# Optimization experiments

Measured on AMD Instinct MI355X. Metric: run time of the kernel, lower is better.

The kernel has to match this reference:

```python
import jax, jax.numpy as jnp
import numpy as np

B, L, D, H, DH, FF = 4, 1024, 1024, 16, 64, 4096
EPS = 1e-5


def _layer_norm(x, g, b):
    m = jnp.mean(x, -1, keepdims=True)
    v = jnp.mean((x - m) ** 2, -1, keepdims=True)
    return (x - m) * jax.lax.rsqrt(v + EPS) * g + b


def setup_inputs() -> dict:
    key = jax.random.key(0)
    ks = jax.random.split(key, 20)
    s = 0.02  # param init scale
    return {
        "x": jax.random.normal(ks[0], (B, L, D), jnp.float32),
        "adj_mask_matrix": jax.random.uniform(ks[1], (B * H, L, L), jnp.float32),
        "com_mask_matrix": jax.random.uniform(ks[2], (B * H, L, L), jnp.float32),
        "lattice_rel": jax.random.normal(ks[3], (2, 1, 1, DH), jnp.float32),
        "Wq": jax.random.normal(ks[4], (D, D), jnp.float32) * s,
        "bq": jnp.zeros((D,), jnp.float32),
        "Wk": jax.random.normal(ks[5], (D, D), jnp.float32) * s,
        "bk": jnp.zeros((D,), jnp.float32),
        "Wv": jax.random.normal(ks[6], (D, D), jnp.float32) * s,
        "bv": jnp.zeros((D,), jnp.float32),
        "Wo": jax.random.normal(ks[7], (D, D), jnp.float32) * s,
        "bo": jnp.zeros((D,), jnp.float32),
        "ln1_scale": jnp.ones((D,), jnp.float32),
        "ln1_bias": jnp.zeros((D,), jnp.float32),
        "W1": jax.random.normal(ks[8], (D, FF), jnp.float32) * s,
        "b1": jnp.zeros((FF,), jnp.float32),
        "W2": jax.random.normal(ks[9], (FF, D), jnp.float32) * s,
        "b2": jnp.zeros((D,), jnp.float32),
        "ln2_scale": jnp.ones((D,), jnp.float32),
        "ln2_bias": jnp.zeros((D,), jnp.float32),
    }


def reference(x, adj_mask_matrix, com_mask_matrix, lattice_rel,
              Wq, bq, Wk, bk, Wv, bv, Wo, bo, ln1_scale, ln1_bias,
              W1, b1, W2, b2, ln2_scale, ln2_bias):
    Bsz, Ln, Dm = x.shape
    # QKV projections; flat reshape [B,L,H*dh] -> [B*H,L,dh] matches torch .view
    Q = (x @ Wq + bq).reshape(Bsz * H, Ln, DH)
    K = (x @ Wk + bk).reshape(Bsz * H, Ln, DH)
    V = (x @ Wv + bv).reshape(Bsz * H, Ln, DH)
    scale = DH ** (-0.5)
    adj_rel = lattice_rel[0]  # [1,1,dh] broadcasts over (B*H, L)
    com_rel = lattice_rel[1]
    att_adj = jnp.einsum('bqd,bkd->bqk', Q + adj_rel, K + adj_rel) * scale
    att_com = jnp.einsum('bqd,bkd->bqk', Q + com_rel, K + com_rel) * scale
    # post-softmax multiplicative masking, then sum of the two attention maps
    mask_att = (jax.nn.softmax(att_adj, axis=-1) * adj_mask_matrix
                + jax.nn.softmax(att_com, axis=-1) * com_mask_matrix)
    context = jnp.matmul(mask_att, V).reshape(Bsz, Ln, H * DH)
    out = _layer_norm(context @ Wo + bo + x, ln1_scale, ln1_bias)
    ff = jax.nn.relu(out @ W1 + b1) @ W2 + b2
    return _layer_norm(ff + out, ln2_scale, ln2_bias)
```

## Files before the change

kernel.cpp:

```cpp
#include <hip/hip_runtime.h>

typedef __attribute__((ext_vector_type(8))) short s16x8;
typedef __attribute__((ext_vector_type(4))) float f32x4;
typedef unsigned short u16;
typedef unsigned int u32;

__device__ __forceinline__ u16 f2b(float f) {
    u32 u = __float_as_uint(f);
    u32 r = (u + 0x7fffu + ((u >> 16) & 1u)) >> 16;
    return (u16)r;
}

#define MFMA16(a, b, c) __builtin_amdgcn_mfma_f32_16x16x32_bf16(a, b, c, 0, 0, 0)
#define GLDS(gp, lp)                                                              \
    __builtin_amdgcn_global_load_lds((const __attribute__((address_space(1))) void*)(gp), \
                                     (__attribute__((address_space(3))) void*)(lp), 16, 0, 0)

__global__ void k_f2b(const float* __restrict__ in, u16* __restrict__ out, int n4) {
    int i = blockIdx.x * 256 + threadIdx.x;
    if (i >= n4) return;
    float4 v = ((const float4*)in)[i];
    ushort4 o;
    o.x = f2b(v.x); o.y = f2b(v.y); o.z = f2b(v.z); o.w = f2b(v.w);
    ((ushort4*)out)[i] = o;
}

__global__ void k_wtrans(const float* __restrict__ W, u16* __restrict__ Wt, int K, int N) {
    __shared__ float t[32][33];
    int bx = blockIdx.x * 32, by = blockIdx.y * 32;
    int tx = threadIdx.x, ty = threadIdx.y;
    for (int i = 0; i < 32; i += 8)
        t[ty + i][tx] = W[(size_t)(by + ty + i) * N + bx + tx];
    __syncthreads();
    for (int i = 0; i < 32; i += 8)
        Wt[(size_t)(bx + ty + i) * K + by + tx] = f2b(t[tx][ty + i]);
}

__global__ __launch_bounds__(256) void gemm_bt(const u16* __restrict__ A, const u16* __restrict__ Bt,
                                               float* __restrict__ C, int M, int N, int K) {
    __shared__ __align__(16) short lA[128 * 64];
    __shared__ __align__(16) short lB[128 * 64];
    const int tid = threadIdx.x, lane = tid & 63, w = tid >> 6;
    const int l15 = lane & 15, lg = lane >> 4;
    const int bm = blockIdx.y, bn = blockIdx.x;
    const int wr = w >> 1, wc = w & 1;
    const int m0 = bm * 128, n0 = bn * 128;
    f32x4 acc[4][4] = {};

    for (int k0 = 0; k0 < K; k0 += 64) {
        #pragma unroll
        for (int i = 0; i < 4; i++) {
            int chunk = w * 4 + i;
            int arow = m0 + chunk * 8 + (lane >> 3);
            GLDS(A + (size_t)arow * K + k0 + (lane & 7) * 8, (short*)lA + chunk * 512);
            int brow = n0 + chunk * 8 + (lane >> 3);
            GLDS(Bt + (size_t)brow * K + k0 + (lane & 7) * 8, (short*)lB + chunk * 512);
        }
        __syncthreads();
        #pragma unroll
        for (int ks = 0; ks < 2; ks++) {
            s16x8 af[4], bfr[4];
            #pragma unroll
            for (int m = 0; m < 4; m++)
                af[m] = *(const s16x8*)&lA[(wr * 64 + m * 16 + l15) * 64 + ks * 32 + lg * 8];
            #pragma unroll
            for (int n = 0; n < 4; n++)
                bfr[n] = *(const s16x8*)&lB[(wc * 64 + n * 16 + l15) * 64 + ks * 32 + lg * 8];
            #pragma unroll
            for (int m = 0; m < 4; m++)
                #pragma unroll
                for (int n = 0; n < 4; n++)
                    acc[m][n] = MFMA16(af[m], bfr[n], acc[m][n]);
        }
        __syncthreads();
    }
    const int rbase = m0 + wr * 64, cbase = n0 + wc * 64;
    #pragma unroll
    for (int m = 0; m < 4; m++)
        #pragma unroll
        for (int n = 0; n < 4; n++) {
            int col = cbase + n * 16 + l15;
            int row0 = rbase + m * 16 + lg * 4;
            #pragma unroll
            for (int r = 0; r < 4; r++)
                C[(size_t)(row0 + r) * N + col] = acc[m][n][r];
        }
}

__global__ void k_epi_qk(const float* __restrict__ Qf, const float* __restrict__ bias,
                         const float* __restrict__ rel, u16* __restrict__ Pa, u16* __restrict__ Pc, int n4) {
    int i = blockIdx.x * 256 + threadIdx.x;
    if (i >= n4) return;
    float4 v = ((const float4*)Qf)[i];
    int c = (i * 4) & 1023;
    int d = (i * 4) & 63;
    float4 b = *(const float4*)(bias + c);
    float4 r0 = *(const float4*)(rel + d);
    float4 r1 = *(const float4*)(rel + 64 + d);
    ushort4 oa, oc;
    oa.x = f2b(v.x + b.x + r0.x); oa.y = f2b(v.y + b.y + r0.y);
    oa.z = f2b(v.z + b.z + r0.z); oa.w = f2b(v.w + b.w + r0.w);
    oc.x = f2b(v.x + b.x + r1.x); oc.y = f2b(v.y + b.y + r1.y);
    oc.z = f2b(v.z + b.z + r1.z); oc.w = f2b(v.w + b.w + r1.w);
    ((ushort4*)Pa)[i] = oa;
    ((ushort4*)Pc)[i] = oc;
}

__global__ void k_vtrans(const float* __restrict__ Vf, const float* __restrict__ bv, u16* __restrict__ Vt) {
    __shared__ float t[64][65];
    const int g = blockIdx.y, lt = blockIdx.x;
    const int tx = threadIdx.x & 63, ty = threadIdx.x >> 6;
    const size_t gQ = (size_t)g * 65536;
    for (int i = 0; i < 64; i += 4) {
        int l = lt * 64 + ty + i;
        t[ty + i][tx] = Vf[gQ + (size_t)l * 64 + tx] + bv[((l & 15) * 64 + tx)];
    }
    __syncthreads();
    for (int i = 0; i < 64; i += 4) {
        int d = ty + i;
        Vt[gQ + (size_t)d * 1024 + lt * 64 + tx] = f2b(t[tx][d]);
    }
}

__global__ __launch_bounds__(256) void k_attn(const u16* __restrict__ Qa, const u16* __restrict__ Qc,
                                              const u16* __restrict__ Ka, const u16* __restrict__ Kc,
                                              const u16* __restrict__ Vt,
                                              const float* __restrict__ adjm, const float* __restrict__ comm,
                                              u16* __restrict__ ctx) {
    const int g = blockIdx.y, qt = blockIdx.x;
    const int tid = threadIdx.x, lane = tid & 63, w = tid >> 6;
    const int l15 = lane & 15, lg = lane >> 4;
    __shared__ __align__(16) short lP[4][2][1024];

    const int q0 = qt * 64 + w * 16;
    const size_t gQ = (size_t)g * 65536;
    const size_t mbase = (size_t)g * 1048576;
    const float scale = 0.125f;

    s16x8 qa[2], qc[2];
    #pragma unroll
    for (int ks = 0; ks < 2; ks++) {
        size_t off = gQ + (size_t)(q0 + l15) * 64 + ks * 32 + lg * 8;
        qa[ks] = *(const s16x8*)(Qa + off);
        qc[ks] = *(const s16x8*)(Qc + off);
    }
    f32x4 ca[4] = {}, cc[4] = {};
    float la[4] = {0.f, 0.f, 0.f, 0.f}, lc[4] = {0.f, 0.f, 0.f, 0.f};

    #pragma unroll 1
    for (int kb = 0; kb < 1024; kb += 64) {
        f32x4 sa[4] = {}, sc[4] = {};
        #pragma unroll
        for (int ks = 0; ks < 2; ks++)
            #pragma unroll
            for (int n = 0; n < 4; n++) {
                size_t koff = gQ + (size_t)(kb + n * 16 + l15) * 64 + ks * 32 + lg * 8;
                s16x8 kfa = *(const s16x8*)(Ka + koff);
                s16x8 kfc = *(const s16x8*)(Kc + koff);
                sa[n] = MFMA16(qa[ks], kfa, sa[n]);
                sc[n] = MFMA16(qc[ks], kfc, sc[n]);
            }
        float suma[4] = {0.f, 0.f, 0.f, 0.f}, sumc[4] = {0.f, 0.f, 0.f, 0.f};
        #pragma unroll
        for (int n = 0; n < 4; n++) {
            int col = kb + n * 16 + l15;
            #pragma unroll
            for (int r = 0; r < 4; r++) {
                int row = q0 + lg * 4 + r;
                float ea = __expf(sa[n][r] * scale);
                float ec = __expf(sc[n][r] * scale);
                suma[r] += ea;
                sumc[r] += ec;
                size_t mi = mbase + (size_t)row * 1024 + col;
                float pa = ea * adjm[mi];
                float pc = ec * comm[mi];
                int lidx = (lg * 4 + r) * 64 + n * 16 + l15;
                lP[w][0][lidx] = (short)f2b(pa);
                lP[w][1][lidx] = (short)f2b(pc);
            }
        }
        #pragma unroll
        for (int r = 0; r < 4; r++) {
            float sA = suma[r], sC = sumc[r];
            #pragma unroll
            for (int m = 8; m >= 1; m >>= 1) {
                sA += __shfl_xor(sA, m);
                sC += __shfl_xor(sC, m);
            }
            la[r] += sA;
            lc[r] += sC;
        }
        #pragma unroll
        for (int ks = 0; ks < 2; ks++) {
            s16x8 pfa = *(const s16x8*)&lP[w][0][l15 * 64 + ks * 32 + lg * 8];
            s16x8 pfc = *(const s16x8*)&lP[w][1][l15 * 64 + ks * 32 + lg * 8];
            #pragma unroll
            for (int d = 0; d < 4; d++) {
                size_t voff = gQ + (size_t)(d * 16 + l15) * 1024 + kb + ks * 32 + lg * 8;
                s16x8 vf = *(const s16x8*)(Vt + voff);
                ca[d] = MFMA16(pfa, vf, ca[d]);
                cc[d] = MFMA16(pfc, vf, cc[d]);
            }
        }
    }
    #pragma unroll
    for (int r = 0; r < 4; r++) {
        float ila = 1.f / la[r], ilc = 1.f / lc[r];
        int row = q0 + lg * 4 + r;
        #pragma unroll
        for (int d = 0; d < 4; d++) {
            float v = ca[d][r] * ila + cc[d][r] * ilc;
            ctx[gQ + (size_t)row * 64 + d * 16 + l15] = f2b(v);
        }
    }
}

__global__ void k_relu_b(const float* __restrict__ in, const float* __restrict__ bias,
                         u16* __restrict__ out, int n4, int ncm1) {
    int i = blockIdx.x * 256 + threadIdx.x;
    if (i >= n4) return;
    float4 v = ((const float4*)in)[i];
    int c = (i * 4) & ncm1;
    float4 b = *(const float4*)(bias + c);
    ushort4 o;
    o.x = f2b(fmaxf(v.x + b.x, 0.f));
    o.y = f2b(fmaxf(v.y + b.y, 0.f));
    o.z = f2b(fmaxf(v.z + b.z, 0.f));
    o.w = f2b(fmaxf(v.w + b.w, 0.f));
    ((ushort4*)out)[i] = o;
}

__global__ __launch_bounds__(256) void k_ln(const float* __restrict__ a, const float* __restrict__ bias,
                                            const float* __restrict__ resid, const float* __restrict__ gamma,
                                            const float* __restrict__ beta, float* __restrict__ out,
                                            u16* __restrict__ outb) {
    const int row = blockIdx.x, tid = threadIdx.x;
    const size_t base = (size_t)row * 1024 + tid * 4;
    float4 av = *(const float4*)(a + base);
    float4 rv = *(const float4*)(resid + base);
    float4 bv = *(const float4*)(bias + tid * 4);
    float t0 = av.x + rv.x + bv.x, t1 = av.y + rv.y + bv.y;
    float t2 = av.z + rv.z + bv.z, t3 = av.w + rv.w + bv.w;
    __shared__ float red[4];
    float s = t0 + t1 + t2 + t3;
    #pragma unroll
    for (int m = 32; m >= 1; m >>= 1) s += __shfl_xor(s, m);
    int w = tid >> 6;
    if ((tid & 63) == 0) red[w] = s;
    __syncthreads();
    float mean = (red[0] + red[1] + red[2] + red[3]) * (1.f / 1024.f);
    float d0 = t0 - mean, d1 = t1 - mean, d2 = t2 - mean, d3 = t3 - mean;
    float q = d0 * d0 + d1 * d1 + d2 * d2 + d3 * d3;
    __syncthreads();
    #pragma unroll
    for (int m = 32; m >= 1; m >>= 1) q += __shfl_xor(q, m);
    if ((tid & 63) == 0) red[w] = q;
    __syncthreads();
    float var = (red[0] + red[1] + red[2] + red[3]) * (1.f / 1024.f);
    float rs = rsqrtf(var + 1e-5f);
    float4 gv = *(const float4*)(gamma + tid * 4);
    float4 bev = *(const float4*)(beta + tid * 4);
    float o0 = d0 * rs * gv.x + bev.x, o1 = d1 * rs * gv.y + bev.y;
    float o2 = d2 * rs * gv.z + bev.z, o3 = d3 * rs * gv.w + bev.w;
    *(float4*)(out + base) = make_float4(o0, o1, o2, o3);
    if (outb) {
        ushort4 ob;
        ob.x = f2b(o0); ob.y = f2b(o1); ob.z = f2b(o2); ob.w = f2b(o3);
        *(ushort4*)(outb + base) = ob;
    }
}

extern "C" void kernel_launch(void* const* d_in, const int* in_sizes, int n_in,
                              void* d_out, int out_size, void* d_ws, size_t ws_size,
                              hipStream_t stream) {
    const float* x    = (const float*)d_in[0];
    const float* adjm = (const float*)d_in[1];
    const float* comm = (const float*)d_in[2];
    const float* rel  = (const float*)d_in[3];
    const float* Wq   = (const float*)d_in[4];
    const float* bq   = (const float*)d_in[5];
    const float* Wk   = (const float*)d_in[6];
    const float* bk   = (const float*)d_in[7];
    const float* Wv   = (const float*)d_in[8];
    const float* bv   = (const float*)d_in[9];
    const float* Wo   = (const float*)d_in[10];
    const float* bo   = (const float*)d_in[11];
    const float* g1   = (const float*)d_in[12];
    const float* be1  = (const float*)d_in[13];
    const float* W1   = (const float*)d_in[14];
    const float* b1   = (const float*)d_in[15];
    const float* W2   = (const float*)d_in[16];
    const float* b2   = (const float*)d_in[17];
    const float* g2   = (const float*)d_in[18];
    const float* be2  = (const float*)d_in[19];
    float* out = (float*)d_out;

    char* ws = (char*)d_ws;
    const size_t MB = 1048576;
    u16*   xb    = (u16*)(ws + 0 * MB);
    u16*   Wqt   = (u16*)(ws + 8 * MB);
    u16*   Wkt   = (u16*)(ws + 10 * MB);
    u16*   Wvt   = (u16*)(ws + 12 * MB);
    u16*   Wot   = (u16*)(ws + 14 * MB);
    u16*   W1t   = (u16*)(ws + 16 * MB);
    u16*   W2t   = (u16*)(ws + 24 * MB);
    float* Qf    = (float*)(ws + 32 * MB);
    float* Kf    = (float*)(ws + 48 * MB);
    float* Vf    = (float*)(ws + 64 * MB);
    u16*   Qab   = (u16*)(ws + 80 * MB);
    u16*   Qcb   = (u16*)(ws + 88 * MB);
    u16*   Kab   = (u16*)(ws + 96 * MB);
    u16*   Kcb   = (u16*)(ws + 104 * MB);
    u16*   Vtb   = (u16*)(ws + 112 * MB);
    u16*   ctx   = (u16*)(ws + 120 * MB);
    float* ctxWo = (float*)(ws + 32 * MB);
    float* out1  = (float*)(ws + 48 * MB);
    u16*   out1b = (u16*)(ws + 64 * MB);
    float* ff1   = (float*)(ws + 80 * MB);
    u16*   rb    = (u16*)(ws + 144 * MB);
    float* ff2   = (float*)(ws + 0 * MB);

    dim3 tb(32, 8);
    k_f2b<<<4096, 256, 0, stream>>>(x, xb, 1048576);
    k_wtrans<<<dim3(32, 32), tb, 0, stream>>>(Wq, Wqt, 1024, 1024);
    k_wtrans<<<dim3(32, 32), tb, 0, stream>>>(Wk, Wkt, 1024, 1024);
    k_wtrans<<<dim3(32, 32), tb, 0, stream>>>(Wv, Wvt, 1024, 1024);
    k_wtrans<<<dim3(32, 32), tb, 0, stream>>>(Wo, Wot, 1024, 1024);
    k_wtrans<<<dim3(128, 32), tb, 0, stream>>>(W1, W1t, 1024, 4096);
    k_wtrans<<<dim3(32, 128), tb, 0, stream>>>(W2, W2t, 4096, 1024);
    gemm_bt<<<dim3(8, 32), 256, 0, stream>>>(xb, Wqt, Qf, 4096, 1024, 1024);
    gemm_bt<<<dim3(8, 32), 256, 0, stream>>>(xb, Wkt, Kf, 4096, 1024, 1024);
    gemm_bt<<<dim3(8, 32), 256, 0, stream>>>(xb, Wvt, Vf, 4096, 1024, 1024);
    k_epi_qk<<<4096, 256, 0, stream>>>(Qf, bq, rel, Qab, Qcb, 1048576);
    k_epi_qk<<<4096, 256, 0, stream>>>(Kf, bk, rel, Kab, Kcb, 1048576);
    k_vtrans<<<dim3(16, 64), 256, 0, stream>>>(Vf, bv, Vtb);
    k_attn<<<dim3(16, 64), 256, 0, stream>>>(Qab, Qcb, Kab, Kcb, Vtb, adjm, comm, ctx);
    gemm_bt<<<dim3(8, 32), 256, 0, stream>>>(ctx, Wot, ctxWo, 4096, 1024, 1024);
    k_ln<<<4096, 256, 0, stream>>>(ctxWo, bo, x, g1, be1, out1, out1b);
    gemm_bt<<<dim3(32, 32), 256, 0, stream>>>(out1b, W1t, ff1, 4096, 4096, 1024);
    k_relu_b<<<16384, 256, 0, stream>>>(ff1, b1, rb, 4194304, 4095);
    gemm_bt<<<dim3(8, 32), 256, 0, stream>>>(rb, W2t, ff2, 4096, 1024, 4096);
    k_ln<<<4096, 256, 0, stream>>>(ff2, b2, out1, g2, be2, out, nullptr);
}
```

Baseline: 657.2 us.

## Fuse QKV GEMM, fold bias+ReLU into FFN1, rework attention masking, smaller-tile GEMM

The three Q/K/V projections become one GEMM over a concatenated transposed weight (N=3072), and the epilogue kernels read from that strided buffer. The FFN1 GEMM now applies bias, ReLU and the bf16 cast in its epilogue, which removes the separate fp32 intermediate and the k_relu_b pass. A 128x64-tile GEMM is added for the N=1024 Wo and W2 GEMMs to put more blocks on the GPU. The attention kernel loads mask rows as vectorized float4 in MFMA operand layout, staging the exps through fp32 LDS, and defers the row-sum shuffles to the end of the loop. This trades extra LDS traffic for coalesced mask loads.

After: 679.1 us. 3.3% more time.

```diff
diff --git a/kernel.cpp b/kernel.cpp
--- a/kernel.cpp
+++ b/kernel.cpp
@@ -1,4 +1,5 @@
 #include <hip/hip_runtime.h>
+#include <hip/hip_bf16.h>
 
 typedef __attribute__((ext_vector_type(8))) short s16x8;
 typedef __attribute__((ext_vector_type(4))) float f32x4;
@@ -9,6 +10,10 @@
     u32 u = __float_as_uint(f);
     u32 r = (u + 0x7fffu + ((u >> 16) & 1u)) >> 16;
     return (u16)r;
+}
+__device__ __forceinline__ u16 bfbits(float f) {
+    __hip_bfloat16 h = __float2bfloat16(f);
+    return *reinterpret_cast<u16*>(&h);
 }
 
 #define MFMA16(a, b, c) __builtin_amdgcn_mfma_f32_16x16x32_bf16(a, b, c, 0, 0, 0)
@@ -36,8 +41,10 @@
         Wt[(size_t)(bx + ty + i) * K + by + tx] = f2b(t[tx][ty + i]);
 }
 
+template <int EPI>
 __global__ __launch_bounds__(256) void gemm_bt(const u16* __restrict__ A, const u16* __restrict__ Bt,
-                                               float* __restrict__ C, int M, int N, int K) {
+                                               void* __restrict__ Cv, int M, int N, int K,
+                                               const float* __restrict__ bias) {
     __shared__ __align__(16) short lA[128 * 64];
     __shared__ __align__(16) short lB[128 * 64];
     const int tid = threadIdx.x, lane = tid & 63, w = tid >> 6;
@@ -81,20 +88,82 @@
         for (int n = 0; n < 4; n++) {
             int col = cbase + n * 16 + l15;
             int row0 = rbase + m * 16 + lg * 4;
+            if (EPI == 0) {
+                float* C = (float*)Cv;
+                #pragma unroll
+                for (int r = 0; r < 4; r++)
+                    C[(size_t)(row0 + r) * N + col] = acc[m][n][r];
+            } else {
+                u16* C = (u16*)Cv;
+                float bv = bias[col];
+                #pragma unroll
+                for (int r = 0; r < 4; r++)
+                    C[(size_t)(row0 + r) * N + col] = bfbits(fmaxf(acc[m][n][r] + bv, 0.f));
+            }
+        }
+}
+
+__global__ __launch_bounds__(256) void gemm_bt64(const u16* __restrict__ A, const u16* __restrict__ Bt,
+                                                 float* __restrict__ C, int M, int N, int K) {
+    __shared__ __align__(16) short lA[128 * 64];
+    __shared__ __align__(16) short lB[64 * 64];
+    const int tid = threadIdx.x, lane = tid & 63, w = tid >> 6;
+    const int l15 = lane & 15, lg = lane >> 4;
+    const int m0 = blockIdx.y * 128, n0 = blockIdx.x * 64;
+    f32x4 acc[2][4] = {};
+
+    for (int k0 = 0; k0 < K; k0 += 64) {
+        #pragma unroll
+        for (int i = 0; i < 4; i++) {
+            int chunk = w * 4 + i;
+            int arow = m0 + chunk * 8 + (lane >> 3);
+            GLDS(A + (size_t)arow * K + k0 + (lane & 7) * 8, (short*)lA + chunk * 512);
+        }
+        #pragma unroll
+        for (int i = 0; i < 2; i++) {
+            int chunk = w * 2 + i;
+            int brow = n0 + chunk * 8 + (lane >> 3);
+            GLDS(Bt + (size_t)brow * K + k0 + (lane & 7) * 8, (short*)lB + chunk * 512);
+        }
+        __syncthreads();
+        #pragma unroll
+        for (int ks = 0; ks < 2; ks++) {
+            s16x8 af[2], bfr[4];
+            #pragma unroll
+            for (int m = 0; m < 2; m++)
+                af[m] = *(const s16x8*)&lA[(w * 32 + m * 16 + l15) * 64 + ks * 32 + lg * 8];
+            #pragma unroll
+            for (int n = 0; n < 4; n++)
+                bfr[n] = *(const s16x8*)&lB[(n * 16 + l15) * 64 + ks * 32 + lg * 8];
+            #pragma unroll
+            for (int m = 0; m < 2; m++)
+                #pragma unroll
+                for (int n = 0; n < 4; n++)
+                    acc[m][n] = MFMA16(af[m], bfr[n], acc[m][n]);
+        }
+        __syncthreads();
+    }
+    #pragma unroll
+    for (int m = 0; m < 2; m++)
+        #pragma unroll
+        for (int n = 0; n < 4; n++) {
+            int col = n0 + n * 16 + l15;
+            int row0 = m0 + w * 32 + m * 16 + lg * 4;
             #pragma unroll
             for (int r = 0; r < 4; r++)
                 C[(size_t)(row0 + r) * N + col] = acc[m][n][r];
         }
 }
 
-__global__ void k_epi_qk(const float* __restrict__ Qf, const float* __restrict__ bias,
-                         const float* __restrict__ rel, u16* __restrict__ Pa, u16* __restrict__ Pc, int n4) {
+__global__ void k_epi_qk2(const float* __restrict__ QKVf, int coff, const float* __restrict__ bias,
+                          const float* __restrict__ rel, u16* __restrict__ Pa, u16* __restrict__ Pc, int n4) {
     int i = blockIdx.x * 256 + threadIdx.x;
     if (i >= n4) return;
-    float4 v = ((const float4*)Qf)[i];
-    int c = (i * 4) & 1023;
-    int d = (i * 4) & 63;
-    float4 b = *(const float4*)(bias + c);
+    int f = i * 4;
+    int row = f >> 10, col = f & 1023;
+    float4 v = *(const float4*)(QKVf + (size_t)row * 3072 + coff + col);
+    int d = f & 63;
+    float4 b = *(const float4*)(bias + col);
     float4 r0 = *(const float4*)(rel + d);
     float4 r1 = *(const float4*)(rel + 64 + d);
     ushort4 oa, oc;
@@ -106,14 +175,15 @@
     ((ushort4*)Pc)[i] = oc;
 }
 
-__global__ void k_vtrans(const float* __restrict__ Vf, const float* __restrict__ bv, u16* __restrict__ Vt) {
+__global__ void k_vtrans2(const float* __restrict__ QKVf, const float* __restrict__ bv, u16* __restrict__ Vt) {
     __shared__ float t[64][65];
     const int g = blockIdx.y, lt = blockIdx.x;
     const int tx = threadIdx.x & 63, ty = threadIdx.x >> 6;
     const size_t gQ = (size_t)g * 65536;
     for (int i = 0; i < 64; i += 4) {
         int l = lt * 64 + ty + i;
-        t[ty + i][tx] = Vf[gQ + (size_t)l * 64 + tx] + bv[((l & 15) * 64 + tx)];
+        size_t f = gQ + (size_t)l * 64 + tx;
+        t[ty + i][tx] = QKVf[(f >> 10) * 3072 + 2048 + (f & 1023)] + bv[f & 1023];
     }
     __syncthreads();
     for (int i = 0; i < 64; i += 4) {
@@ -130,11 +200,11 @@
     const int g = blockIdx.y, qt = blockIdx.x;
     const int tid = threadIdx.x, lane = tid & 63, w = tid >> 6;
     const int l15 = lane & 15, lg = lane >> 4;
-    __shared__ __align__(16) short lP[4][2][1024];
+    __shared__ __align__(16) float lE[4][2][16][68];
 
     const int q0 = qt * 64 + w * 16;
     const size_t gQ = (size_t)g * 65536;
-    const size_t mbase = (size_t)g * 1048576;
+    const size_t mrow = (size_t)g * 1048576 + (size_t)(q0 + l15) * 1024;
     const float scale = 0.125f;
 
     s16x8 qa[2], qc[2];
@@ -149,6 +219,16 @@
 
     #pragma unroll 1
     for (int kb = 0; kb < 1024; kb += 64) {
+        float4 maf[2][2], mcf[2][2];
+        #pragma unroll
+        for (int ks = 0; ks < 2; ks++) {
+            const float* pa_ = adjm + mrow + kb + ks * 32 + lg * 8;
+            const float* pc_ = comm + mrow + kb + ks * 32 + lg * 8;
+            maf[ks][0] = *(const float4*)pa_;
+            maf[ks][1] = *(const float4*)(pa_ + 4);
+            mcf[ks][0] = *(const float4*)pc_;
+            mcf[ks][1] = *(const float4*)(pc_ + 4);
+        }
         f32x4 sa[4] = {}, sc[4] = {};
         #pragma unroll
         for (int ks = 0; ks < 2; ks++)
@@ -160,47 +240,46 @@
                 sa[n] = MFMA16(qa[ks], kfa, sa[n]);
                 sc[n] = MFMA16(qc[ks], kfc, sc[n]);
             }
-        float suma[4] = {0.f, 0.f, 0.f, 0.f}, sumc[4] = {0.f, 0.f, 0.f, 0.f};
-        #pragma unroll
-        for (int n = 0; n < 4; n++) {
-            int col = kb + n * 16 + l15;
+        #pragma unroll
+        for (int n = 0; n < 4; n++)
             #pragma unroll
             for (int r = 0; r < 4; r++) {
-                int row = q0 + lg * 4 + r;
                 float ea = __expf(sa[n][r] * scale);
                 float ec = __expf(sc[n][r] * scale);
-                suma[r] += ea;
-                sumc[r] += ec;
-                size_t mi = mbase + (size_t)row * 1024 + col;
-                float pa = ea * adjm[mi];
-                float pc = ec * comm[mi];
-                int lidx = (lg * 4 + r) * 64 + n * 16 + l15;
-                lP[w][0][lidx] = (short)f2b(pa);
-                lP[w][1][lidx] = (short)f2b(pc);
+                la[r] += ea;
+                lc[r] += ec;
+                lE[w][0][lg * 4 + r][n * 16 + l15] = ea;
+                lE[w][1][lg * 4 + r][n * 16 + l15] = ec;
             }
-        }
-        #pragma unroll
-        for (int r = 0; r < 4; r++) {
-            float sA = suma[r], sC = sumc[r];
-            #pragma unroll
-            for (int m = 8; m >= 1; m >>= 1) {
-                sA += __shfl_xor(sA, m);
-                sC += __shfl_xor(sC, m);
+        #pragma unroll
+        for (int ks = 0; ks < 2; ks++) {
+            const float* ea_p = &lE[w][0][l15][ks * 32 + lg * 8];
+            const float* ec_p = &lE[w][1][l15][ks * 32 + lg * 8];
+            float4 e0 = *(const float4*)ea_p, e1 = *(const float4*)(ea_p + 4);
+            float4 f0 = *(const float4*)ec_p, f1 = *(const float4*)(ec_p + 4);
+            union { s16x8 v; u16 u[8]; } pA, pC;
+            pA.u[0] = bfbits(e0.x * maf[ks][0].x); pA.u[1] = bfbits(e0.y * maf[ks][0].y);
+            pA.u[2] = bfbits(e0.z * maf[ks][0].z); pA.u[3] = bfbits(e0.w * maf[ks][0].w);
+            pA.u[4] = bfbits(e1.x * maf[ks][1].x); pA.u[5] = bfbits(e1.y * maf[ks][1].y);
+            pA.u[6] = bfbits(e1.z * maf[ks][1].z); pA.u[7] = bfbits(e1.w * maf[ks][1].w);
+            pC.u[0] = bfbits(f0.x * mcf[ks][0].x); pC.u[1] = bfbits(f0.y * mcf[ks][0].y);
+            pC.u[2] = bfbits(f0.z * mcf[ks][0].z); pC.u[3] = bfbits(f0.w * mcf[ks][0].w);
+            pC.u[4] = bfbits(f1.x * mcf[ks][1].x); pC.u[5] = bfbits(f1.y * mcf[ks][1].y);
+            pC.u[6] = bfbits(f1.z * mcf[ks][1].z); pC.u[7] = bfbits(f1.w * mcf[ks][1].w);
+            #pragma unroll
+            for (int d = 0; d < 4; d++) {
+                s16x8 vf = *(const s16x8*)(Vt + gQ + (size_t)(d * 16 + l15) * 1024 + kb + ks * 32 + lg * 8);
+                ca[d] = MFMA16(pA.v, vf, ca[d]);
+                cc[d] = MFMA16(pC.v, vf, cc[d]);
             }
-            la[r] += sA;
-            lc[r] += sC;
-        }
-        #pragma unroll
-        for (int ks = 0; ks < 2; ks++) {
-            s16x8 pfa = *(const s16x8*)&lP[w][0][l15 * 64 + ks * 32 + lg * 8];
-            s16x8 pfc = *(const s16x8*)&lP[w][1][l15 * 64 + ks * 32 + lg * 8];
-            #pragma unroll
-            for (int d = 0; d < 4; d++) {
-                size_t voff = gQ + (size_t)(d * 16 + l15) * 1024 + kb + ks * 32 + lg * 8;
-                s16x8 vf = *(const s16x8*)(Vt + voff);
-                ca[d] = MFMA16(pfa, vf, ca[d]);
-                cc[d] = MFMA16(pfc, vf, cc[d]);
-            }
+        }
+    }
+    #pragma unroll
+    for (int r = 0; r < 4; r++) {
+        #pragma unroll
+        for (int m = 8; m >= 1; m >>= 1) {
+            la[r] += __shfl_xor(la[r], m);
+            lc[r] += __shfl_xor(lc[r], m);
         }
     }
     #pragma unroll
@@ -213,21 +292,6 @@
             ctx[gQ + (size_t)row * 64 + d * 16 + l15] = f2b(v);
         }
     }
-}
-
-__global__ void k_relu_b(const float* __restrict__ in, const float* __restrict__ bias,
-                         u16* __restrict__ out, int n4, int ncm1) {
-    int i = blockIdx.x * 256 + threadIdx.x;
-    if (i >= n4) return;
-    float4 v = ((const float4*)in)[i];
-    int c = (i * 4) & ncm1;
-    float4 b = *(const float4*)(bias + c);
-    ushort4 o;
-    o.x = f2b(fmaxf(v.x + b.x, 0.f));
-    o.y = f2b(fmaxf(v.y + b.y, 0.f));
-    o.z = f2b(fmaxf(v.z + b.z, 0.f));
-    o.w = f2b(fmaxf(v.w + b.w, 0.f));
-    ((ushort4*)out)[i] = o;
 }
 
 __global__ __launch_bounds__(256) void k_ln(const float* __restrict__ a, const float* __restrict__ bias,
@@ -298,15 +362,11 @@
     char* ws = (char*)d_ws;
     const size_t MB = 1048576;
     u16*   xb    = (u16*)(ws + 0 * MB);
-    u16*   Wqt   = (u16*)(ws + 8 * MB);
-    u16*   Wkt   = (u16*)(ws + 10 * MB);
-    u16*   Wvt   = (u16*)(ws + 12 * MB);
+    u16*   Wqkvt = (u16*)(ws + 8 * MB);
     u16*   Wot   = (u16*)(ws + 14 * MB);
     u16*   W1t   = (u16*)(ws + 16 * MB);
     u16*   W2t   = (u16*)(ws + 24 * MB);
-    float* Qf    = (float*)(ws + 32 * MB);
-    float* Kf    = (float*)(ws + 48 * MB);
-    float* Vf    = (float*)(ws + 64 * MB);
+    float* QKVf  = (float*)(ws + 32 * MB);
     u16*   Qab   = (u16*)(ws + 80 * MB);
     u16*   Qcb   = (u16*)(ws + 88 * MB);
     u16*   Kab   = (u16*)(ws + 96 * MB);
@@ -316,29 +376,25 @@
     float* ctxWo = (float*)(ws + 32 * MB);
     float* out1  = (float*)(ws + 48 * MB);
     u16*   out1b = (u16*)(ws + 64 * MB);
-    float* ff1   = (float*)(ws + 80 * MB);
-    u16*   rb    = (u16*)(ws + 144 * MB);
+    u16*   rb    = (u16*)(ws + 80 * MB);
     float* ff2   = (float*)(ws + 0 * MB);
 
     dim3 tb(32, 8);
     k_f2b<<<4096, 256, 0, stream>>>(x, xb, 1048576);
-    k_wtrans<<<dim3(32, 32), tb, 0, stream>>>(Wq, Wqt, 1024, 1024);
-    k_wtrans<<<dim3(32, 32), tb, 0, stream>>>(Wk, Wkt, 1024, 1024);
-    k_wtrans<<<dim3(32, 32), tb, 0, stream>>>(Wv, Wvt, 1024, 1024);
+    k_wtrans<<<dim3(32, 32), tb, 0, stream>>>(Wq, Wqkvt, 1024, 1024);
+    k_wtrans<<<dim3(32, 32), tb, 0, stream>>>(Wk, Wqkvt + 1024 * 1024, 1024, 1024);
+    k_wtrans<<<dim3(32, 32), tb, 0, stream>>>(Wv, Wqkvt + 2 * 1024 * 1024, 1024, 1024);
     k_wtrans<<<dim3(32, 32), tb, 0, stream>>>(Wo, Wot, 1024, 1024);
     k_wtrans<<<dim3(128, 32), tb, 0, stream>>>(W1, W1t, 1024, 4096);
     k_wtrans<<<dim3(32, 128), tb, 0, stream>>>(W2, W2t, 4096, 1024);
-    gemm_bt<<<dim3(8, 32), 256, 0, stream>>>(xb, Wqt, Qf, 4096, 1024, 1024);
-    gemm_bt<<<dim3(8, 32), 256, 0, stream>>>(xb, Wkt, Kf, 4096, 1024, 1024);
-    gemm_bt<<<dim3(8, 32), 256, 0, stream>>>(xb, Wvt, Vf, 4096, 1024, 1024);
-    k_epi_qk<<<4096, 256, 0, stream>>>(Qf, bq, rel, Qab, Qcb, 1048576);
-    k_epi_qk<<<4096, 256, 0, stream>>>(Kf, bk, rel, Kab, Kcb, 1048576);
-    k_vtrans<<<dim3(16, 64), 256, 0, stream>>>(Vf, bv, Vtb);
+    gemm_bt<0><<<dim3(24, 32), 256, 0, stream>>>(xb, Wqkvt, QKVf, 4096, 3072, 1024, nullptr);
+    k_epi_qk2<<<4096, 256, 0, stream>>>(QKVf, 0, bq, rel, Qab, Qcb, 1048576);
+    k_epi_qk2<<<4096, 256, 0, stream>>>(QKVf, 1024, bk, rel, Kab, Kcb, 1048576);
+    k_vtrans2<<<dim3(16, 64), 256, 0, stream>>>(QKVf, bv, Vtb);
     k_attn<<<dim3(16, 64), 256, 0, stream>>>(Qab, Qcb, Kab, Kcb, Vtb, adjm, comm, ctx);
-    gemm_bt<<<dim3(8, 32), 256, 0, stream>>>(ctx, Wot, ctxWo, 4096, 1024, 1024);
+    gemm_bt64<<<dim3(16, 32), 256, 0, stream>>>(ctx, Wot, ctxWo, 4096, 1024, 1024);
     k_ln<<<4096, 256, 0, stream>>>(ctxWo, bo, x, g1, be1, out1, out1b);
-    gemm_bt<<<dim3(32, 32), 256, 0, stream>>>(out1b, W1t, ff1, 4096, 4096, 1024);
-    k_relu_b<<<16384, 256, 0, stream>>>(ff1, b1, rb, 4194304, 4095);
-    gemm_bt<<<dim3(8, 32), 256, 0, stream>>>(rb, W2t, ff2, 4096, 1024, 4096);
+    gemm_bt<1><<<dim3(32, 32), 256, 0, stream>>>(out1b, W1t, rb, 4096, 4096, 1024, b1);
+    gemm_bt64<<<dim3(16, 32), 256, 0, stream>>>(rb, W2t, ff2, 4096, 1024, 4096);
     k_ln<<<4096, 256, 0, stream>>>(ff2, b2, out1, g2, be2, out, nullptr);
 }
```
